# Optimization experiments

Measured on AMD Instinct MI355X. Metric: run time of the kernel, lower is better.

The kernel has to match this reference:

```python
import jax, jax.numpy as jnp
import numpy as np

BN_EPS = 1e-5


def setup_inputs() -> dict:
    key = jax.random.key(0)
    ks = jax.random.split(key, 9)
    N, C, T, V, S, INTER, OUT = 64, 64, 300, 25, 3, 16, 64
    return {
        "x": jax.random.normal(ks[0], (N, C, T, V), dtype=jnp.float32),
        "A": jax.random.uniform(ks[1], (S, V, V), dtype=jnp.float32),
        "PA": jax.random.normal(ks[2], (S, V, V), dtype=jnp.float32) * 1e-3,
        "Wa": jax.random.normal(ks[3], (S, INTER, C), dtype=jnp.float32) * 0.1,
        "ba": jax.random.normal(ks[4], (S, INTER), dtype=jnp.float32) * 0.1,
        "Wb": jax.random.normal(ks[5], (S, INTER, C), dtype=jnp.float32) * 0.1,
        "bb": jax.random.normal(ks[6], (S, INTER), dtype=jnp.float32) * 0.1,
        "Wd": jax.random.normal(ks[7], (S, OUT, C), dtype=jnp.float32) * 0.1,
        "bd": jax.random.normal(ks[8], (S, OUT), dtype=jnp.float32) * 0.1,
        "gamma": jnp.ones((OUT,), dtype=jnp.float32),
        "beta": jnp.zeros((OUT,), dtype=jnp.float32),
    }


def reference(x, A, PA, Wa, ba, Wb, bb, Wd, bd, gamma, beta):
    N, C, T, V = x.shape
    S, INTER = Wa.shape[0], Wa.shape[1]
    K = INTER * T  # contraction length for attention

    # 1x1 convs for all subsets at once: [N,S,inter,T,V]
    fa = jnp.einsum('nctv,sic->nsitv', x, Wa) + ba[None, :, :, None, None]
    fb = jnp.einsum('nctv,sic->nsitv', x, Wb) + bb[None, :, :, None, None]

    # A1: permute(0,3,1,2).view(N,V,inter*T)  -> [N,S,V,K]
    A1 = fa.transpose(0, 1, 4, 2, 3).reshape(N, S, V, K)
    # A2: view(N,inter*T,V)                   -> [N,S,K,V]
    A2 = fb.reshape(N, S, K, V)

    # attention: softmax over dim=-2, plus learned adjacency
    att = jnp.einsum('nsvk,nskw->nsvw', A1, A2) / jnp.asarray(K, x.dtype)
    att = jax.nn.softmax(att, axis=-2) + (A + PA)[None]  # [N,S,V,V]

    # message passing: x.view(N,C*T,V) @ att, then 1x1 conv_d, summed over subsets
    xm = jnp.einsum('nkv,nsvw->nskw', x.reshape(N, C * T, V), att)
    xm = xm.reshape(N, S, C, T, V)
    y = jnp.einsum('nsctv,soc->notv', xm, Wd) + bd.sum(0)[None, :, None, None]

    # BatchNorm2d (training-mode batch stats, per-channel over N,T,V)
    mean = y.mean(axis=(0, 2, 3), keepdims=True)
    var = y.var(axis=(0, 2, 3), keepdims=True)
    y = gamma[None, :, None, None] * (y - mean) * jax.lax.rsqrt(var + BN_EPS) \
        + beta[None, :, None, None]

    # residual (in_channels == out_channels -> identity down) + relu
    return jax.nn.relu(y + x)
```

## Files before the change

### kernel.cpp

```cpp
#include <hip/hip_runtime.h>
#include <math.h>

constexpr int Nn = 64, Cc = 64, Tt = 300, Vv = 25, Ss = 3, Ii = 16, Oo = 64;
constexpr int TVc  = Tt * Vv;
constexpr int CTVc = Cc * TVc;
constexpr float KINV = 1.0f / 4800.0f;

constexpr int WS_ATT  = 0;
constexpr int WS_SUM  = 120000;
constexpr int WS_SQ   = 120064;
constexpr int WS_MEAN = 120128;
constexpr int WS_RSTD = 120192;
constexpr int WS_ZERO_FLOATS = 120128;

typedef __attribute__((ext_vector_type(8))) short bf16x8;
typedef __attribute__((ext_vector_type(4))) short short4v;
typedef __attribute__((ext_vector_type(4))) float f32x4;
typedef __attribute__((ext_vector_type(16))) float f32x16;
typedef __attribute__((ext_vector_type(4))) int int4v;

__device__ __forceinline__ short f2bf(float f) {
    unsigned u = __builtin_bit_cast(unsigned, f);
    u += 0x7FFFu + ((u >> 16) & 1u);
    return (short)(u >> 16);
}
__device__ __forceinline__ float bf2f(short s) {
    unsigned u = ((unsigned)(unsigned short)s) << 16;
    return __builtin_bit_cast(float, u);
}
__device__ __forceinline__ void store4(float* p, f32x4 v) {
    __builtin_memcpy(p, &v, 16);
}

__global__ __launch_bounds__(256) void ka_gram_mfma(
    const float* __restrict__ x,
    const float* __restrict__ Wa, const float* __restrict__ ba,
    const float* __restrict__ Wb, const float* __restrict__ bb,
    float* __restrict__ att)
{
    __shared__ short uT[112 * 104];
    __shared__ float part[4 * 1024];
    __shared__ float bab[96];

    const int tid = threadIdx.x;
    const int t0  = blockIdx.x * 4;
    const int n   = blockIdx.y;
    const float* xn = x + n * CTVc + t0 * 25;

    if (tid < 96) {
        const int s = tid >> 5, r = tid & 31;
        bab[tid] = (r < 16) ? ba[s * 16 + r] : bb[s * 16 + r - 16];
    }

    const int lane = tid & 63;
    const int wave = tid >> 6;
    const int l16  = lane & 15;
    const int quad = lane >> 4;

    bf16x8 afr[3][2][2];
    #pragma unroll
    for (int s = 0; s < 3; ++s)
        #pragma unroll
        for (int half = 0; half < 2; ++half)
            #pragma unroll
            for (int k = 0; k < 2; ++k) {
                const float* W = half ? Wb : Wa;
                const float* wp = W + (s * 16 + l16) * 64 + k * 32 + quad * 8;
                const float4 w0 = *(const float4*)wp;
                const float4 w1 = *(const float4*)(wp + 4);
                bf16x8 a;
                a[0] = f2bf(w0.x); a[1] = f2bf(w0.y); a[2] = f2bf(w0.z); a[3] = f2bf(w0.w);
                a[4] = f2bf(w1.x); a[5] = f2bf(w1.y); a[6] = f2bf(w1.z); a[7] = f2bf(w1.w);
                afr[s][half][k] = a;
            }
    __syncthreads();

    for (int nt = wave; nt < 7; nt += 4) {
        const int tv = nt * 16 + l16;
        const bool ok = tv < 100;
        const float* bp = xn + (quad * 8) * 7500 + tv;
        bf16x8 b0, b1;
        #pragma unroll
        for (int j = 0; j < 8; ++j) {
            const float f0 = ok ? bp[j * 7500] : 0.0f;
            const float f1 = ok ? bp[(j + 32) * 7500] : 0.0f;
            b0[j] = f2bf(f0);
            b1[j] = f2bf(f1);
        }
        #pragma unroll
        for (int s = 0; s < 3; ++s)
            #pragma unroll
            for (int half = 0; half < 2; ++half) {
                f32x4 acc = {0.0f, 0.0f, 0.0f, 0.0f};
                acc = __builtin_amdgcn_mfma_f32_16x16x32_bf16(afr[s][half][0], b0, acc, 0, 0, 0);
                acc = __builtin_amdgcn_mfma_f32_16x16x32_bf16(afr[s][half][1], b1, acc, 0, 0, 0);
                const float4 bv = *(const float4*)(bab + s * 32 + half * 16 + quad * 4);
                short4v pk;
                pk[0] = f2bf(acc[0] + bv.x); pk[1] = f2bf(acc[1] + bv.y);
                pk[2] = f2bf(acc[2] + bv.z); pk[3] = f2bf(acc[3] + bv.w);
                *(short4v*)(uT + tv * 104 + s * 32 + half * 16 + quad * 4) = pk;
            }
    }
    __syncthreads();

    const int t   = wave;
    const int w32 = lane & 31;
    const int khi = lane >> 5;
    f32x16 g[3];
    #pragma unroll
    for (int s = 0; s < 3; ++s)
        #pragma unroll
        for (int r = 0; r < 16; ++r) g[s][r] = 0.0f;

    #pragma unroll
    for (int s = 0; s < 3; ++s) {
        const short* base = uT + (t * 25 + w32) * 104 + s * 32 + khi * 8;
        const bf16x8 aA = *(const bf16x8*)(base);
        const bf16x8 bB = *(const bf16x8*)(base + 16);
        g[s] = __builtin_amdgcn_mfma_f32_32x32x16_bf16(aA, bB, g[s], 0, 0, 0);
    }

    for (int s = 0; s < 3; ++s) {
        __syncthreads();
        #pragma unroll
        for (int r = 0; r < 16; ++r) {
            const int row = (r & 3) + 8 * (r >> 2) + 4 * khi;
            part[wave * 1024 + row * 32 + w32] = g[s][r];
        }
        __syncthreads();
        float* attns = att + (n * 3 + s) * 625;
        for (int p = tid; p < 625; p += 256) {
            const int v = p / 25, w = p - v * 25;
            const int q = v * 32 + w;
            atomicAdd(attns + p, part[q] + part[1024 + q] + part[2048 + q] + part[3072 + q]);
        }
    }
}

__global__ __launch_bounds__(64) void kb_softmax(
    float* __restrict__ att, const float* __restrict__ A, const float* __restrict__ PA)
{
    const int b = blockIdx.x;
    const int s = b % 3;
    const int w = threadIdx.x;
    if (w >= 25) return;
    float* base = att + b * 625;
    float col[25];
    float m = -1e30f;
    #pragma unroll
    for (int v = 0; v < 25; ++v) {
        col[v] = base[v * 25 + w] * KINV;
        m = fmaxf(m, col[v]);
    }
    float sum = 0.0f;
    #pragma unroll
    for (int v = 0; v < 25; ++v) { col[v] = expf(col[v] - m); sum += col[v]; }
    const float inv = 1.0f / sum;
    #pragma unroll
    for (int v = 0; v < 25; ++v)
        base[v * 25 + w] = fmaf(col[v], inv, A[(s * 25 + v) * 25 + w] + PA[(s * 25 + v) * 25 + w]);
}

__global__ __launch_bounds__(256) void k3_y_mfma(
    const float* __restrict__ x, const float* __restrict__ Wd,
    const float* __restrict__ att, float* __restrict__ y, float* __restrict__ bns)
{
    __shared__ __align__(16) short U[96 * 128];
    __shared__ __align__(16) short attT[3 * 1024];
    __shared__ float bn1[4][32], bn2[4][32];

    const int tid = threadIdx.x;
    const int t0  = blockIdx.x * 4;
    const int n   = blockIdx.y;
    const int oh  = blockIdx.z;
    const float* xn = x + n * CTVc + t0 * 25;

    const int lane = tid & 63;
    const int wave = tid >> 6;
    const int l16  = lane & 15;
    const int quad = lane >> 4;

    for (int i = tid; i < 1536; i += 256)
        ((int4v*)U)[i] = (int4v){0, 0, 0, 0};

    for (int i = tid; i < 3072; i += 256) {
        const int s = i >> 10, r = i & 1023, v = r >> 5, vp = r & 31;
        const float val = (v < 25 && vp < 25) ? att[(n * 3 + s) * 625 + vp * 25 + v] : 0.0f;
        attT[i] = f2bf(val);
    }

    bf16x8 afr[3][2][2];
    #pragma unroll
    for (int s = 0; s < 3; ++s)
        #pragma unroll
        for (int m = 0; m < 2; ++m)
            #pragma unroll
            for (int k = 0; k < 2; ++k) {
                const float* wp = Wd + ((s * 64 + oh * 32 + m * 16 + l16) * 64) + k * 32 + quad * 8;
                const float4 w0 = *(const float4*)wp;
                const float4 w1 = *(const float4*)(wp + 4);
                bf16x8 a;
                a[0] = f2bf(w0.x); a[1] = f2bf(w0.y); a[2] = f2bf(w0.z); a[3] = f2bf(w0.w);
                a[4] = f2bf(w1.x); a[5] = f2bf(w1.y); a[6] = f2bf(w1.z); a[7] = f2bf(w1.w);
                afr[s][m][k] = a;
            }
    __syncthreads();

    for (int nt = wave; nt < 7; nt += 4) {
        const int tv = nt * 16 + l16;
        const bool ok = tv < 100;
        const float* bp = xn + (quad * 8) * 7500 + tv;
        bf16x8 b0, b1;
        #pragma unroll
        for (int j = 0; j < 8; ++j) {
            const float f0 = ok ? bp[j * 7500] : 0.0f;
            const float f1 = ok ? bp[(j + 32) * 7500] : 0.0f;
            b0[j] = f2bf(f0);
            b1[j] = f2bf(f1);
        }
        const int tl  = tv / 25;
        const int vp  = tv - tl * 25;
        const int col = tl * 32 + vp;
        const int grp = col >> 3, ing = col & 7;
        #pragma unroll
        for (int s = 0; s < 3; ++s)
            #pragma unroll
            for (int m = 0; m < 2; ++m) {
                f32x4 acc = {0.0f, 0.0f, 0.0f, 0.0f};
                acc = __builtin_amdgcn_mfma_f32_16x16x32_bf16(afr[s][m][0], b0, acc, 0, 0, 0);
                acc = __builtin_amdgcn_mfma_f32_16x16x32_bf16(afr[s][m][1], b1, acc, 0, 0, 0);
                if (ok) {
                    #pragma unroll
                    for (int r = 0; r < 4; ++r) {
                        const int row = s * 32 + m * 16 + quad * 4 + r;
                        U[row * 128 + (((grp ^ (row & 15)) << 3) | ing)] = f2bf(acc[r]);
                    }
                }
            }
    }
    __syncthreads();

    const int t = wave;
    bf16x8 aF[3][2], bF[3][2];
    #pragma unroll
    for (int s = 0; s < 3; ++s) {
        #pragma unroll
        for (int mt = 0; mt < 2; ++mt)
            aF[s][mt] = *(const bf16x8*)(attT + s * 1024 + (mt * 16 + l16) * 32 + quad * 8);
        #pragma unroll
        for (int nb = 0; nb < 2; ++nb) {
            const int row = s * 32 + nb * 16 + l16;
            bF[s][nb] = *(const bf16x8*)(U + row * 128 + (((t * 4 + quad) ^ (row & 15)) << 3));
        }
    }
    f32x4 D[2][2];
    #pragma unroll
    for (int mt = 0; mt < 2; ++mt)
        #pragma unroll
        for (int nb = 0; nb < 2; ++nb) D[mt][nb] = (f32x4){0.0f, 0.0f, 0.0f, 0.0f};
    #pragma unroll
    for (int s = 0; s < 3; ++s)
        #pragma unroll
        for (int mt = 0; mt < 2; ++mt)
            #pragma unroll
            for (int nb = 0; nb < 2; ++nb)
                D[mt][nb] = __builtin_amdgcn_mfma_f32_16x16x32_bf16(aF[s][mt], bF[s][nb], D[mt][nb], 0, 0, 0);

    float s1[2] = {0.0f, 0.0f}, s2[2] = {0.0f, 0.0f};
    #pragma unroll
    for (int nb = 0; nb < 2; ++nb) {
        const int og = oh * 32 + nb * 16 + l16;
        float* dst = y + ((size_t)(n * 64 + og) * 300 + t0 + t) * 25;
        const f32x4 d0 = D[0][nb];
        store4(dst + quad * 4, d0);
        s1[nb] += d0[0] + d0[1] + d0[2] + d0[3];
        s2[nb] += d0[0]*d0[0] + d0[1]*d0[1] + d0[2]*d0[2] + d0[3]*d0[3];
        const f32x4 d1 = D[1][nb];
        if (quad < 2) {
            store4(dst + 16 + quad * 4, d1);
            s1[nb] += d1[0] + d1[1] + d1[2] + d1[3];
            s2[nb] += d1[0]*d1[0] + d1[1]*d1[1] + d1[2]*d1[2] + d1[3]*d1[3];
        } else if (quad == 2) {
            dst[24] = d1[0];
            s1[nb] += d1[0];
            s2[nb] += d1[0] * d1[0];
        }
    }
    #pragma unroll
    for (int nb = 0; nb < 2; ++nb) {
        s1[nb] += __shfl_xor(s1[nb], 16); s1[nb] += __shfl_xor(s1[nb], 32);
        s2[nb] += __shfl_xor(s2[nb], 16); s2[nb] += __shfl_xor(s2[nb], 32);
    }
    if (lane < 16) {
        bn1[wave][lane]      = s1[0];
        bn1[wave][16 + lane] = s1[1];
        bn2[wave][lane]      = s2[0];
        bn2[wave][16 + lane] = s2[1];
    }
    __syncthreads();
    if (tid < 32) {
        const float S1 = bn1[0][tid] + bn1[1][tid] + bn1[2][tid] + bn1[3][tid];
        const float S2 = bn2[0][tid] + bn2[1][tid] + bn2[2][tid] + bn2[3][tid];
        atomicAdd(bns + oh * 32 + tid, S1);
        atomicAdd(bns + 64 + oh * 32 + tid, S2);
    }
}

__global__ __launch_bounds__(64) void k3b_stats(float* __restrict__ ws)
{
    const int o = threadIdx.x;
    if (o >= 64) return;
    const float cnt_inv = 1.0f / 480000.0f;
    const float s = ws[WS_SUM + o], q = ws[WS_SQ + o];
    const float mean = s * cnt_inv;
    const float var  = q * cnt_inv - mean * mean;
    ws[WS_MEAN + o] = mean;
    ws[WS_RSTD + o] = rsqrtf(var + 1e-5f);
}

__global__ __launch_bounds__(256) void k4_bn(
    float* __restrict__ out, const float* __restrict__ x,
    const float* __restrict__ gamma, const float* __restrict__ beta,
    const float* __restrict__ ws)
{
    const int i4 = blockIdx.x * 256 + threadIdx.x;
    const int o = (i4 / 1875) & 63;
    const float mean = ws[WS_MEAN + o], rstd = ws[WS_RSTD + o];
    const float g = gamma[o], b = beta[o];
    const float4 yv = ((const float4*)out)[i4];
    const float4 xv = ((const float4*)x)[i4];
    float4 r;
    r.x = fmaxf(fmaf(g * (yv.x - mean), rstd, b) + xv.x, 0.0f);
    r.y = fmaxf(fmaf(g * (yv.y - mean), rstd, b) + xv.y, 0.0f);
    r.z = fmaxf(fmaf(g * (yv.z - mean), rstd, b) + xv.z, 0.0f);
    r.w = fmaxf(fmaf(g * (yv.w - mean), rstd, b) + xv.w, 0.0f);
    ((float4*)out)[i4] = r;
}

extern "C" void kernel_launch(void* const* d_in, const int* in_sizes, int n_in,
                              void* d_out, int out_size, void* d_ws, size_t ws_size,
                              hipStream_t stream)
{
    const float* x  = (const float*)d_in[0];
    const float* A  = (const float*)d_in[1];
    const float* PA = (const float*)d_in[2];
    const float* Wa = (const float*)d_in[3];
    const float* ba = (const float*)d_in[4];
    const float* Wb = (const float*)d_in[5];
    const float* bb = (const float*)d_in[6];
    const float* Wd = (const float*)d_in[7];
    const float* gamma = (const float*)d_in[9];
    const float* beta  = (const float*)d_in[10];
    float* out = (float*)d_out;
    float* ws  = (float*)d_ws;

    hipMemsetAsync(d_ws, 0, (size_t)WS_ZERO_FLOATS * sizeof(float), stream);
    ka_gram_mfma<<<dim3(75, 64), 256, 0, stream>>>(x, Wa, ba, Wb, bb, ws + WS_ATT);
    kb_softmax<<<dim3(192), 64, 0, stream>>>(ws + WS_ATT, A, PA);
    k3_y_mfma<<<dim3(75, 64, 2), 256, 0, stream>>>(x, Wd, ws + WS_ATT, out, ws + WS_SUM);
    k3b_stats<<<dim3(1), 64, 0, stream>>>(ws);
    k4_bn<<<dim3(30000), 256, 0, stream>>>(out, x, gamma, beta, ws);
}
```

Before: 521.0 us.

## Pre-transpose x into channel-last bf16 buffer shared by gram and output kernels

Adds a pre-pass kernel that converts x to bf16 and transposes it to [N, T*V, C] in workspace. The gram and output MFMA kernels then load B fragments as contiguous 16-byte vectors instead of eight strided fp32 loads with per-element conversion. The goal is to cut strided global traffic and conversion work in two kernels that each read all of x (three block reads in total). The cost is an extra kernel that reads x and writes a ~61 MB bf16 copy, and the new path only runs when the workspace is large enough.

```diff
diff --git a/kernel.cpp b/kernel.cpp
--- a/kernel.cpp
+++ b/kernel.cpp
@@ -12,6 +12,9 @@
 constexpr int WS_MEAN = 120128;
 constexpr int WS_RSTD = 120192;
 constexpr int WS_ZERO_FLOATS = 120128;
+constexpr int WS_XB_F = 120256;
+constexpr size_t XB_BYTES = (size_t)Nn * TVc * Cc * 2;
+constexpr size_t WS_NEED  = (size_t)WS_XB_F * 4 + XB_BYTES;
 
 typedef __attribute__((ext_vector_type(8))) short bf16x8;
 typedef __attribute__((ext_vector_type(4))) short short4v;
@@ -32,8 +35,43 @@
     __builtin_memcpy(p, &v, 16);
 }
 
+__global__ __launch_bounds__(256) void k0_xpose(
+    const float* __restrict__ x, short* __restrict__ xb)
+{
+    const int n   = blockIdx.y;
+    const int tid = threadIdx.x;
+    const int tv  = blockIdx.x * 32 + (tid & 31);
+    const int g   = (tid >> 5) & 7;
+    if (tv >= TVc) return;
+    const float* xp = x + (size_t)n * CTVc + (size_t)(g * 8) * TVc + tv;
+    bf16x8 o;
+    #pragma unroll
+    for (int j = 0; j < 8; ++j) o[j] = f2bf(xp[(size_t)j * TVc]);
+    *(bf16x8*)(xb + ((size_t)n * TVc + tv) * 64 + g * 8) = o;
+}
+
+template<bool XB>
+__device__ __forceinline__ void load_xfrag(
+    const float* __restrict__ xn, const short* __restrict__ xbn,
+    int tv, bool ok, int quad, bf16x8& b0, bf16x8& b1)
+{
+    if constexpr (XB) {
+        const short* bp = xbn + (ok ? tv : 0) * 64 + quad * 8;
+        b0 = *(const bf16x8*)bp;
+        b1 = *(const bf16x8*)(bp + 32);
+    } else {
+        const float* bp = xn + (quad * 8) * TVc + tv;
+        #pragma unroll
+        for (int j = 0; j < 8; ++j) {
+            b0[j] = f2bf(ok ? bp[j * TVc] : 0.0f);
+            b1[j] = f2bf(ok ? bp[(j + 32) * TVc] : 0.0f);
+        }
+    }
+}
+
+template<bool XB>
 __global__ __launch_bounds__(256) void ka_gram_mfma(
-    const float* __restrict__ x,
+    const float* __restrict__ x, const short* __restrict__ xb,
     const float* __restrict__ Wa, const float* __restrict__ ba,
     const float* __restrict__ Wb, const float* __restrict__ bb,
     float* __restrict__ att)
@@ -45,7 +83,8 @@
     const int tid = threadIdx.x;
     const int t0  = blockIdx.x * 4;
     const int n   = blockIdx.y;
-    const float* xn = x + n * CTVc + t0 * 25;
+    const float* xn  = x + n * CTVc + t0 * 25;
+    const short* xbn = XB ? (xb + ((size_t)n * TVc + t0 * 25) * 64) : nullptr;
 
     if (tid < 96) {
         const int s = tid >> 5, r = tid & 31;
@@ -78,15 +117,8 @@
     for (int nt = wave; nt < 7; nt += 4) {
         const int tv = nt * 16 + l16;
         const bool ok = tv < 100;
-        const float* bp = xn + (quad * 8) * 7500 + tv;
         bf16x8 b0, b1;
-        #pragma unroll
-        for (int j = 0; j < 8; ++j) {
-            const float f0 = ok ? bp[j * 7500] : 0.0f;
-            const float f1 = ok ? bp[(j + 32) * 7500] : 0.0f;
-            b0[j] = f2bf(f0);
-            b1[j] = f2bf(f1);
-        }
+        load_xfrag<XB>(xn, xbn, tv, ok, quad, b0, b1);
         #pragma unroll
         for (int s = 0; s < 3; ++s)
             #pragma unroll
@@ -161,8 +193,10 @@
         base[v * 25 + w] = fmaf(col[v], inv, A[(s * 25 + v) * 25 + w] + PA[(s * 25 + v) * 25 + w]);
 }
 
+template<bool XB>
 __global__ __launch_bounds__(256) void k3_y_mfma(
-    const float* __restrict__ x, const float* __restrict__ Wd,
+    const float* __restrict__ x, const short* __restrict__ xb,
+    const float* __restrict__ Wd,
     const float* __restrict__ att, float* __restrict__ y, float* __restrict__ bns)
 {
     __shared__ __align__(16) short U[96 * 128];
@@ -173,7 +207,8 @@
     const int t0  = blockIdx.x * 4;
     const int n   = blockIdx.y;
     const int oh  = blockIdx.z;
-    const float* xn = x + n * CTVc + t0 * 25;
+    const float* xn  = x + n * CTVc + t0 * 25;
+    const short* xbn = XB ? (xb + ((size_t)n * TVc + t0 * 25) * 64) : nullptr;
 
     const int lane = tid & 63;
     const int wave = tid >> 6;
@@ -209,15 +244,8 @@
     for (int nt = wave; nt < 7; nt += 4) {
         const int tv = nt * 16 + l16;
         const bool ok = tv < 100;
-        const float* bp = xn + (quad * 8) * 7500 + tv;
         bf16x8 b0, b1;
-        #pragma unroll
-        for (int j = 0; j < 8; ++j) {
-            const float f0 = ok ? bp[j * 7500] : 0.0f;
-            const float f1 = ok ? bp[(j + 32) * 7500] : 0.0f;
-            b0[j] = f2bf(f0);
-            b1[j] = f2bf(f1);
-        }
+        load_xfrag<XB>(xn, xbn, tv, ok, quad, b0, b1);
         const int tl  = tv / 25;
         const int vp  = tv - tl * 25;
         const int col = tl * 32 + vp;
@@ -355,9 +383,18 @@
     float* ws  = (float*)d_ws;
 
     hipMemsetAsync(d_ws, 0, (size_t)WS_ZERO_FLOATS * sizeof(float), stream);
-    ka_gram_mfma<<<dim3(75, 64), 256, 0, stream>>>(x, Wa, ba, Wb, bb, ws + WS_ATT);
-    kb_softmax<<<dim3(192), 64, 0, stream>>>(ws + WS_ATT, A, PA);
-    k3_y_mfma<<<dim3(75, 64, 2), 256, 0, stream>>>(x, Wd, ws + WS_ATT, out, ws + WS_SUM);
+
+    if (ws_size >= WS_NEED) {
+        short* xb = (short*)(ws + WS_XB_F);
+        k0_xpose<<<dim3(235, 64), 256, 0, stream>>>(x, xb);
+        ka_gram_mfma<true><<<dim3(75, 64), 256, 0, stream>>>(x, xb, Wa, ba, Wb, bb, ws + WS_ATT);
+        kb_softmax<<<dim3(192), 64, 0, stream>>>(ws + WS_ATT, A, PA);
+        k3_y_mfma<true><<<dim3(75, 64, 2), 256, 0, stream>>>(x, xb, Wd, ws + WS_ATT, out, ws + WS_SUM);
+    } else {
+        ka_gram_mfma<false><<<dim3(75, 64), 256, 0, stream>>>(x, nullptr, Wa, ba, Wb, bb, ws + WS_ATT);
+        kb_softmax<<<dim3(192), 64, 0, stream>>>(ws + WS_ATT, A, PA);
+        k3_y_mfma<false><<<dim3(75, 64, 2), 256, 0, stream>>>(x, nullptr, Wd, ws + WS_ATT, out, ws + WS_SUM);
+    }
     k3b_stats<<<dim3(1), 64, 0, stream>>>(ws);
     k4_bn<<<dim3(30000), 256, 0, stream>>>(out, x, gamma, beta, ws);
 }
```

Result: slower. 560.5 us (+7.6%).
